# Kernel tuning notes

Hardware: AMD Instinct MI355X
Metric: run time of the kernel (lower is better)

Reference implementation:

```python
import jax, jax.numpy as jnp
import numpy as np

DIM = 256; DIM_HEAD = 32; HEADS = DIM // DIM_HEAD; WSZ = 8; D4 = DIM // 4
EPS = 1e-5
SCALE = DIM_HEAD ** -0.5


def _rel_pos_indices(wsz):
    pos = np.arange(wsz)
    grid = np.stack(np.meshgrid(pos, pos, indexing='ij')).reshape(2, -1).T  # (w*w, 2)
    rel = grid[:, None] - grid[None, :] + wsz - 1
    return jnp.asarray((rel * np.array([2 * wsz - 1, 1])).sum(-1))  # (w*w, w*w)


def _ln(x, g, b):
    m = x.mean(-1, keepdims=True)
    v = jnp.var(x, axis=-1, keepdims=True)
    return (x - m) / jnp.sqrt(v + EPS) * g + b


def setup_inputs() -> dict:
    key = jax.random.key(0)
    ks = jax.random.split(key, 8)
    inner = HEADS * DIM_HEAD
    def n(k, shape, s=0.02):
        return jax.random.normal(k, shape, dtype=jnp.float32) * s
    return {
        "x": jax.random.normal(ks[0], (2, DIM, 256, 256), dtype=jnp.float32),
        "norm_g": jnp.ones((1, DIM, 1, 1), jnp.float32),
        "norm_b": jnp.zeros((1, DIM, 1, 1), jnp.float32),
        "w_qkv": n(ks[1], (3 * inner, DIM)),
        "w_out": n(ks[2], (DIM, inner)),
        "b_out": jnp.zeros((DIM,), jnp.float32),
        "dpb_w1": n(ks[3], (D4, 2), 0.5), "dpb_b1": jnp.zeros((D4,), jnp.float32),
        "dpb_g1": jnp.ones((D4,), jnp.float32), "dpb_beta1": jnp.zeros((D4,), jnp.float32),
        "dpb_w2": n(ks[4], (D4, D4), 0.1), "dpb_b2": jnp.zeros((D4,), jnp.float32),
        "dpb_g2": jnp.ones((D4,), jnp.float32), "dpb_beta2": jnp.zeros((D4,), jnp.float32),
        "dpb_w3": n(ks[5], (D4, D4), 0.1), "dpb_b3": jnp.zeros((D4,), jnp.float32),
        "dpb_g3": jnp.ones((D4,), jnp.float32), "dpb_beta3": jnp.zeros((D4,), jnp.float32),
        "dpb_w4": n(ks[6], (1, D4), 0.1), "dpb_b4": jnp.zeros((1,), jnp.float32),
    }


def reference(x, norm_g, norm_b, w_qkv, w_out, b_out,
              dpb_w1, dpb_b1, dpb_g1, dpb_beta1,
              dpb_w2, dpb_b2, dpb_g2, dpb_beta2,
              dpb_w3, dpb_b3, dpb_g3, dpb_beta3,
              dpb_w4, dpb_b4):
    B, D, H, W = x.shape
    nh, nw = H // WSZ, W // WSZ
    # channel-first LayerNorm (stats over dim=1, biased variance)
    mean = x.mean(axis=1, keepdims=True)
    var = jnp.var(x, axis=1, keepdims=True)
    xn = (x - mean) / jnp.sqrt(var + EPS) * norm_g + norm_b
    # 'short' windowing: b d (h s1) (w s2) -> (b h w) d (s1 s2)
    xw = xn.reshape(B, D, nh, WSZ, nw, WSZ).transpose(0, 2, 4, 1, 3, 5)
    xw = xw.reshape(B * nh * nw, D, WSZ * WSZ)
    # 1x1 conv QKV == matmul over channel dim
    qkv = jnp.einsum('ed,bdn->ben', w_qkv, xw)
    q, k, v = jnp.split(qkv, 3, axis=1)
    to_heads = lambda t: t.reshape(-1, HEADS, DIM_HEAD, WSZ * WSZ).transpose(0, 1, 3, 2)
    q, k, v = to_heads(q) * SCALE, to_heads(k), to_heads(v)
    sim = jnp.einsum('bhid,bhjd->bhij', q, k)  # [Bw, H, 64, 64]
    # dynamic position bias MLP over relative coordinates in [-wsz, wsz]
    pos = jnp.arange(-WSZ, WSZ + 1, dtype=x.dtype)
    rel = jnp.stack(jnp.meshgrid(pos, pos, indexing='ij')).reshape(2, -1).T  # ((2w+1)^2, 2)
    h1 = jax.nn.relu(_ln(rel @ dpb_w1.T + dpb_b1, dpb_g1, dpb_beta1))
    h2 = jax.nn.relu(_ln(h1 @ dpb_w2.T + dpb_b2, dpb_g2, dpb_beta2))
    h3 = jax.nn.relu(_ln(h2 @ dpb_w3.T + dpb_b3, dpb_g3, dpb_beta3))
    biases = (h3 @ dpb_w4.T + dpb_b4)[:, 0]
    sim = sim + biases[_rel_pos_indices(WSZ)]
    attn = jax.nn.softmax(sim, axis=-1)
    out = jnp.einsum('bhij,bhjd->bhid', attn, v)
    # b h (x y) d -> b (h d) (x y)
    out = out.transpose(0, 1, 3, 2).reshape(-1, HEADS * DIM_HEAD, WSZ * WSZ)
    out = jnp.einsum('de,ben->bdn', w_out, out) + b_out[None, :, None]
    # (b h w) d s1 s2 -> b d (h s1) (w s2)
    out = out.reshape(B, nh, nw, D, WSZ, WSZ).transpose(0, 3, 1, 4, 2, 5).reshape(B, D, H, W)
    return out
```

## Files before the change

kernel.cpp:

```cpp
#include <hip/hip_runtime.h>


typedef __attribute__((ext_vector_type(8))) short bf16x8;
typedef __attribute__((ext_vector_type(4))) short bf16x4;
typedef __attribute__((ext_vector_type(4))) float f32x4;

#define LOG2E    1.44269504088896f
#define QK_SCALE 0.17677669529663687f

__device__ __forceinline__ short f2b(float f) {
  union { float f; unsigned u; } v; v.f = f;
  unsigned r = v.u + 0x7FFFu + ((v.u >> 16) & 1u);
  return (short)(r >> 16);
}

__device__ __forceinline__ unsigned pk2(float a, float b) {
  union { float f; unsigned u; } ua, ub; ua.f = a; ub.f = b;
#if __has_builtin(__builtin_amdgcn_perm)
  return __builtin_amdgcn_perm(ub.u + 0x8000u, ua.u + 0x8000u, 0x07060302u);
#else
  return ((ua.u + 0x8000u) >> 16) | ((ub.u + 0x8000u) & 0xFFFF0000u);
#endif
}

__device__ __forceinline__ bf16x8 mk8(unsigned a, unsigned b, unsigned c, unsigned d) {
  union { unsigned u[4]; bf16x8 v; } x; x.u[0] = a; x.u[1] = b; x.u[2] = c; x.u[3] = d;
  return x.v;
}
__device__ __forceinline__ bf16x4 mk4(unsigned a, unsigned b) {
  union { unsigned u[2]; bf16x4 v; } x; x.u[0] = a; x.u[1] = b; return x.v;
}

__device__ __forceinline__ f32x4 mfma16(bf16x4 a, bf16x4 b, f32x4 c) {
#if __has_builtin(__builtin_amdgcn_mfma_f32_16x16x16bf16_1k)
  return __builtin_amdgcn_mfma_f32_16x16x16bf16_1k(a, b, c, 0, 0, 0);
#else
  f32x4 d;
  asm volatile("v_mfma_f32_16x16x16_bf16 %0, %1, %2, %3"
               : "=&v"(d) : "v"(a), "v"(b), "v"(c));
  return d;
#endif
}

__global__ __launch_bounds__(256)
void wconv_kernel(const float* __restrict__ wqkv, const float* __restrict__ wout,
                  short* __restrict__ wq_t, short* __restrict__ wo_t) {
  int t = (blockIdx.x * 256 + threadIdx.x) * 8;
  if (t < 196608) {
    int blk = t >> 9, l = (t & 511) >> 3;
    int et = blk >> 3, kt = blk & 7;
    int e = et * 16 + (l & 15);
    int d = kt * 32 + (l >> 4) * 8;
    const float* src = wqkv + e * 256 + d;
    float sc = (e < 256) ? QK_SCALE * LOG2E : 1.0f;
    bf16x8 pk;
    #pragma unroll
    for (int el = 0; el < 8; ++el) pk[el] = f2b(src[el] * sc);
    *(bf16x8*)(wq_t + t) = pk;
  } else if (t < 262144) {
    int o = t - 196608;
    int blk = o >> 9, l = (o & 511) >> 3;
    int dt = blk >> 3, kt = blk & 7;
    int dout = dt * 16 + (l & 15);
    int e = kt * 32 + (l >> 4) * 8;
    const float* src = wout + dout * 256 + e;
    bf16x8 pk;
    #pragma unroll
    for (int el = 0; el < 8; ++el) pk[el] = f2b(src[el]);
    *(bf16x8*)(wo_t + o) = pk;
  }
}

__device__ __forceinline__ float wave_sum64(float v) {
  v += __shfl_xor(v, 1);  v += __shfl_xor(v, 2);  v += __shfl_xor(v, 4);
  v += __shfl_xor(v, 8);  v += __shfl_xor(v, 16); v += __shfl_xor(v, 32);
  return v;
}

__global__ __launch_bounds__(64)
void dpb_kernel(const float* __restrict__ w1, const float* __restrict__ b1,
                const float* __restrict__ g1, const float* __restrict__ be1,
                const float* __restrict__ w2, const float* __restrict__ b2,
                const float* __restrict__ g2, const float* __restrict__ be2,
                const float* __restrict__ w3, const float* __restrict__ b3,
                const float* __restrict__ g3, const float* __restrict__ be3,
                const float* __restrict__ w4, const float* __restrict__ b4,
                float* __restrict__ sb) {
  __shared__ float h[64];
  __shared__ float wbuf[4096];
  const int f = threadIdx.x;
  const int pos = blockIdx.x;
  const float py = (float)(pos / 17) - 8.0f;
  const float px = (float)(pos % 17) - 8.0f;

  float a = py * w1[2 * f] + px * w1[2 * f + 1] + b1[f];
  {
    float m = wave_sum64(a) * (1.f / 64.f);
    float d = a - m;
    float var = wave_sum64(d * d) * (1.f / 64.f);
    a = fmaxf(d * rsqrtf(var + 1e-5f) * g1[f] + be1[f], 0.f);
  }
  h[f] = a;
  __threadfence_block();

  #pragma unroll 8
  for (int k = 0; k < 64; ++k) wbuf[k * 64 + f] = w2[k * 64 + f];
  __threadfence_block();
  float acc = b2[f];
  #pragma unroll 8
  for (int k = 0; k < 64; ++k) {
    int g = (k + f) & 63;
    acc += wbuf[f * 64 + g] * h[g];
  }
  {
    float m = wave_sum64(acc) * (1.f / 64.f);
    float d = acc - m;
    float var = wave_sum64(d * d) * (1.f / 64.f);
    acc = fmaxf(d * rsqrtf(var + 1e-5f) * g2[f] + be2[f], 0.f);
  }
  __threadfence_block();
  h[f] = acc;
  __threadfence_block();

  #pragma unroll 8
  for (int k = 0; k < 64; ++k) wbuf[k * 64 + f] = w3[k * 64 + f];
  __threadfence_block();
  float acc3 = b3[f];
  #pragma unroll 8
  for (int k = 0; k < 64; ++k) {
    int g = (k + f) & 63;
    acc3 += wbuf[f * 64 + g] * h[g];
  }
  {
    float m = wave_sum64(acc3) * (1.f / 64.f);
    float d = acc3 - m;
    float var = wave_sum64(d * d) * (1.f / 64.f);
    acc3 = fmaxf(d * rsqrtf(var + 1e-5f) * g3[f] + be3[f], 0.f);
  }
  float o = wave_sum64(w4[f] * acc3);
  if (f == 0) sb[pos] = o + b4[0];
}

__global__ __launch_bounds__(512)
void expand_kernel(const float* __restrict__ sb, float* __restrict__ tblf) {
  int idx = blockIdx.x * 512 + threadIdx.x;
  int it = idx >> 10, jt = (idx >> 8) & 3, ln = (idx >> 2) & 63, jj = idx & 3;
  int rr = ln & 15, gg = ln >> 4;
  int i = it * 16 + rr;
  int j = jt * 16 + gg * 4 + jj;
  int dy = (i >> 3) - (j >> 3) + 7;
  int dx = (i & 7) - (j & 7) + 7;
  tblf[idx] = sb[dy * 15 + dx] * LOG2E;
}

#define SM_XA   0
#define SM_PS   65536
#define SM_SIZE 73728
#define XASWZ(p) ((((p) & 7) << 4) ^ ((((p) >> 3) & 3) << 7))

__global__ __launch_bounds__(512)
void attn_kernel(const float* __restrict__ x, const float* __restrict__ gnorm,
                 const float* __restrict__ bnorm, const short* __restrict__ wq_t,
                 const short* __restrict__ wo_t, const float* __restrict__ bout,
                 const float* __restrict__ tblf, float* __restrict__ out) {
  __shared__ __align__(16) char smem[SM_SIZE];
  const int t = threadIdx.x;
  const int lane = t & 63;
  const int w = t >> 6;
  const int r = lane & 15;
  const int gq = lane >> 4;

  const int bid = blockIdx.x;
  const int b   = bid >> 9;
  const int wh  = (bid >> 4) & 31;
  const int ww2 = bid & 15;
  const int R = wh * 8, C = ww2 * 16;

  const int n = lane;
  const int d0 = w * 32;
  float* PS = (float*)(smem + SM_PS);
  float xv[2][32];
  #pragma unroll
  for (int h = 0; h < 2; ++h) {
    const float* xb = x + (((size_t)(b * 256 + d0)) << 16) +
                      (R + 4 * h + (n >> 4)) * 256 + C + (n & 15);
    float s1 = 0.f, s2v = 0.f;
    #pragma unroll
    for (int i = 0; i < 32; ++i) {
      float v = xb[(size_t)i << 16];
      xv[h][i] = v; s1 += v; s2v += v * v;
    }
    PS[h * 1024 + w * 64 + n] = s1;
    PS[h * 1024 + 512 + w * 64 + n] = s2v;
  }
  __syncthreads();
  #pragma unroll
  for (int h = 0; h < 2; ++h) {
    float a = 0.f, q2 = 0.f;
    #pragma unroll
    for (int dg = 0; dg < 8; ++dg) {
      a  += PS[h * 1024 + dg * 64 + n];
      q2 += PS[h * 1024 + 512 + dg * 64 + n];
    }
    float mean = a * (1.f / 256.f);
    float var = q2 * (1.f / 256.f) - mean * mean;
    float rstd = rsqrtf(var + 1e-5f);
    int p2 = (4 * h + (n >> 4)) * 16 + (n & 15);
    #pragma unroll
    for (int c = 0; c < 4; ++c) {
      float xn[8];
      #pragma unroll
      for (int e = 0; e < 8; ++e) {
        int d = d0 + c * 8 + e;
        xn[e] = (xv[h][c * 8 + e] - mean) * rstd * gnorm[d] + bnorm[d];
      }
      *(bf16x8*)(smem + SM_XA + (p2 << 9) + ((((d0 + c * 8) << 1)) ^ XASWZ(p2))) =
          mk8(pk2(xn[0], xn[1]), pk2(xn[2], xn[3]), pk2(xn[4], xn[5]), pk2(xn[6], xn[7]));
    }
  }
  __syncthreads();

  const f32x4 vzero = {0.f, 0.f, 0.f, 0.f};

  #define QKV_SWAP(PP, ACC)                                                     \
    {                                                                           \
      _Pragma("unroll")                                                         \
      for (int nt = 0; nt < 2; ++nt)                                            \
        _Pragma("unroll")                                                       \
        for (int t4 = 0; t4 < 4; ++t4) ACC[nt][t4] = vzero;                     \
      _Pragma("unroll")                                                         \
      for (int kt = 0; kt < 8; ++kt) {                                          \
        bf16x8 bfr0 = *(const bf16x8*)(wq_t + (((((PP) * 16 + w * 2 + 0) * 8 + kt) << 9) + lane * 8)); \
        bf16x8 bfr1 = *(const bf16x8*)(wq_t + (((((PP) * 16 + w * 2 + 1) * 8 + kt) << 9) + lane * 8)); \
        bf16x8 afr[4];                                                          \
        _Pragma("unroll")                                                       \
        for (int t4 = 0; t4 < 4; ++t4) {                                        \
          int p2 = (t4 * 2 + (r >> 3)) * 16 + wl * 8 + (r & 7);                 \
          afr[t4] = *(const bf16x8*)(smem + SM_XA + (p2 << 9) + ((((kt * 32 + gq * 8) << 1)) ^ XASWZ(p2))); \
        }                                                                       \
        _Pragma("unroll")                                                       \
        for (int t4 = 0; t4 < 4; ++t4) {                                        \
          ACC[0][t4] = __builtin_amdgcn_mfma_f32_16x16x32_bf16(bfr0, afr[t4], ACC[0][t4], 0, 0, 0); \
          ACC[1][t4] = __builtin_amdgcn_mfma_f32_16x16x32_bf16(bfr1, afr[t4], ACC[1][t4], 0, 0, 0); \
        }                                                                       \
      }                                                                         \
    }

  f32x4 o2[2][2][4];
  #pragma unroll
  for (int wl = 0; wl < 2; ++wl) {
    bf16x4 kpk[2][4], qpk[2][4];
    {
      f32x4 acc[2][4];
      QKV_SWAP(1, acc);
      #pragma unroll
      for (int kb = 0; kb < 2; ++kb)
        #pragma unroll
        for (int jt = 0; jt < 4; ++jt)
          kpk[kb][jt] = mk4(pk2(acc[kb][jt][0], acc[kb][jt][1]),
                            pk2(acc[kb][jt][2], acc[kb][jt][3]));
    }
    {
      f32x4 acc[2][4];
      QKV_SWAP(0, acc);
      #pragma unroll
      for (int kb = 0; kb < 2; ++kb)
        #pragma unroll
        for (int it = 0; it < 4; ++it)
          qpk[kb][it] = mk4(pk2(acc[kb][it][0], acc[kb][it][1]),
                            pk2(acc[kb][it][2], acc[kb][it][3]));
    }
    bf16x4 va8[4][2];
    {
      f32x4 vacc[4][2];
      #pragma unroll
      for (int mt = 0; mt < 4; ++mt)
        #pragma unroll
        for (int nt = 0; nt < 2; ++nt) vacc[mt][nt] = vzero;
      #pragma unroll
      for (int kt = 0; kt < 8; ++kt) {
        bf16x8 bfr0 = *(const bf16x8*)(wq_t + ((((2 * 16 + w * 2 + 0) * 8 + kt) << 9) + lane * 8));
        bf16x8 bfr1 = *(const bf16x8*)(wq_t + ((((2 * 16 + w * 2 + 1) * 8 + kt) << 9) + lane * 8));
        bf16x8 afr[4];
        #pragma unroll
        for (int mt = 0; mt < 4; ++mt) {
          int p2 = (mt * 2 + (r >> 3)) * 16 + wl * 8 + (r & 7);
          afr[mt] = *(const bf16x8*)(smem + SM_XA + (p2 << 9) + ((((kt * 32 + gq * 8) << 1)) ^ XASWZ(p2)));
        }
        #pragma unroll
        for (int mt = 0; mt < 4; ++mt) {
          vacc[mt][0] = __builtin_amdgcn_mfma_f32_16x16x32_bf16(afr[mt], bfr0, vacc[mt][0], 0, 0, 0);
          vacc[mt][1] = __builtin_amdgcn_mfma_f32_16x16x32_bf16(afr[mt], bfr1, vacc[mt][1], 0, 0, 0);
        }
      }
      #pragma unroll
      for (int mt = 0; mt < 4; ++mt)
        #pragma unroll
        for (int nt = 0; nt < 2; ++nt)
          va8[mt][nt] = mk4(pk2(vacc[mt][nt][0], vacc[mt][nt][1]),
                            pk2(vacc[mt][nt][2], vacc[mt][nt][3]));
    }

    #pragma unroll
    for (int nt = 0; nt < 2; ++nt)
      #pragma unroll
      for (int it = 0; it < 4; ++it) o2[wl][nt][it] = vzero;
    __builtin_amdgcn_s_setprio(1);
    #pragma unroll
    for (int it = 0; it < 4; ++it) {
      f32x4 sc[4];
      #pragma unroll
      for (int jt = 0; jt < 4; ++jt) {
        sc[jt] = mfma16(kpk[0][jt], qpk[0][it], vzero);
        sc[jt] = mfma16(kpk[1][jt], qpk[1][it], sc[jt]);
      }
      float m0 = -1e30f;
      #pragma unroll
      for (int jt = 0; jt < 4; ++jt) {
        f32x4 bj = *(const f32x4*)(tblf + (((it * 4 + jt) * 64 + lane) << 2));
        #pragma unroll
        for (int jj = 0; jj < 4; ++jj) {
          sc[jt][jj] += bj[jj];
          m0 = fmaxf(m0, sc[jt][jj]);
        }
      }
      m0 = fmaxf(m0, __shfl_xor(m0, 16));
      m0 = fmaxf(m0, __shfl_xor(m0, 32));
      float sum = 0.f;
      #pragma unroll
      for (int jt = 0; jt < 4; ++jt)
        #pragma unroll
        for (int jj = 0; jj < 4; ++jj) {
          float e = exp2f(sc[jt][jj] - m0);
          sc[jt][jj] = e; sum += e;
        }
      sum += __shfl_xor(sum, 16);
      sum += __shfl_xor(sum, 32);
      float pinv = 1.0f / sum;
      bf16x4 ppk[4];
      #pragma unroll
      for (int jt = 0; jt < 4; ++jt)
        ppk[jt] = mk4(pk2(sc[jt][0] * pinv, sc[jt][1] * pinv),
                      pk2(sc[jt][2] * pinv, sc[jt][3] * pinv));
      #pragma unroll
      for (int mt = 0; mt < 4; ++mt)
        #pragma unroll
        for (int nt = 0; nt < 2; ++nt)
          o2[wl][nt][it] = mfma16(va8[mt][nt], ppk[mt], o2[wl][nt][it]);
    }
    __builtin_amdgcn_s_setprio(0);
  }
  __syncthreads();

  #pragma unroll
  for (int wl = 0; wl < 2; ++wl)
    #pragma unroll
    for (int nt = 0; nt < 2; ++nt)
      #pragma unroll
      for (int it = 0; it < 4; ++it) {
        int pw = it * 16 + r;
        int p2 = ((pw >> 3) << 4) + (wl << 3) + (pw & 7);
        int e = (w << 5) + (nt << 4) + (gq << 2);
        *(bf16x4*)(smem + SM_XA + (p2 << 9) + (((e << 1)) ^ XASWZ(p2))) =
            mk4(pk2(o2[wl][nt][it][0], o2[wl][nt][it][1]),
                pk2(o2[wl][nt][it][2], o2[wl][nt][it][3]));
      }
  __syncthreads();

  float bov[2];
  bov[0] = bout[w * 32 + r];
  bov[1] = bout[w * 32 + 16 + r];

  #pragma unroll
  for (int ck = 0; ck < 2; ++ck) {
    f32x4 c3[4][2];
    #pragma unroll
    for (int mt = 0; mt < 4; ++mt)
      #pragma unroll
      for (int nt = 0; nt < 2; ++nt) c3[mt][nt] = vzero;
    __builtin_amdgcn_s_setprio(1);
    #pragma unroll
    for (int kt = 0; kt < 8; ++kt) {
      bf16x8 woB[2];
      #pragma unroll
      for (int nt = 0; nt < 2; ++nt)
        woB[nt] = *(const bf16x8*)(wo_t + ((((w * 2 + nt) * 8 + kt) << 9) + lane * 8));
      bf16x8 af[4];
      #pragma unroll
      for (int mt = 0; mt < 4; ++mt) {
        int p2 = ck * 64 + mt * 16 + r;
        af[mt] = *(const bf16x8*)(smem + SM_XA + (p2 << 9) + ((((kt * 32 + gq * 8) << 1)) ^ XASWZ(p2)));
      }
      #pragma unroll
      for (int mt = 0; mt < 4; ++mt)
        #pragma unroll
        for (int nt = 0; nt < 2; ++nt)
          c3[mt][nt] = __builtin_amdgcn_mfma_f32_16x16x32_bf16(af[mt], woB[nt], c3[mt][nt], 0, 0, 0);
    }
    __builtin_amdgcn_s_setprio(0);
    #pragma unroll
    for (int mt = 0; mt < 4; ++mt)
      #pragma unroll
      for (int nt = 0; nt < 2; ++nt) {
        int dout = w * 32 + nt * 16 + r;
        int row = ck * 4 + mt;
        f32x4 v = c3[mt][nt];
        v[0] += bov[nt]; v[1] += bov[nt]; v[2] += bov[nt]; v[3] += bov[nt];
        *(f32x4*)(out + (((size_t)(b * 256 + dout)) << 16) + (R + row) * 256 + C + gq * 4) = v;
      }
  }
  #undef QKV_SWAP
}

extern "C" void kernel_launch(void* const* d_in, const int* in_sizes, int n_in,
                              void* d_out, int out_size, void* d_ws, size_t ws_size,
                              hipStream_t stream) {
  const float* x     = (const float*)d_in[0];
  const float* gnorm = (const float*)d_in[1];
  const float* bnorm = (const float*)d_in[2];
  const float* wqkv  = (const float*)d_in[3];
  const float* wout  = (const float*)d_in[4];
  const float* bout  = (const float*)d_in[5];
  const float* w1  = (const float*)d_in[6];
  const float* b1  = (const float*)d_in[7];
  const float* g1  = (const float*)d_in[8];
  const float* be1 = (const float*)d_in[9];
  const float* w2  = (const float*)d_in[10];
  const float* b2  = (const float*)d_in[11];
  const float* g2  = (const float*)d_in[12];
  const float* be2 = (const float*)d_in[13];
  const float* w3  = (const float*)d_in[14];
  const float* b3  = (const float*)d_in[15];
  const float* g3  = (const float*)d_in[16];
  const float* be3 = (const float*)d_in[17];
  const float* w4  = (const float*)d_in[18];
  const float* b4  = (const float*)d_in[19];

  short* wq_t = (short*)d_ws;
  short* wo_t = wq_t + 196608;
  float* sb   = (float*)((char*)d_ws + 524288);
  float* tblf = (float*)((char*)d_ws + 528384);

  wconv_kernel<<<dim3(128), dim3(256), 0, stream>>>(wqkv, wout, wq_t, wo_t);
  dpb_kernel<<<dim3(289), dim3(64), 0, stream>>>(
      w1, b1, g1, be1, w2, b2, g2, be2, w3, b3, g3, be3, w4, b4, sb);
  expand_kernel<<<dim3(8), dim3(512), 0, stream>>>(sb, tblf);

  attn_kernel<<<dim3(1024), dim3(512), 0, stream>>>(
      x, gnorm, bnorm, wq_t, wo_t, bout, tblf, (float*)d_out);
}
```

Before: 193.5 us.

## Split LayerNorm into separate kernel staging swizzled bf16 tiles in workspace

Moves the channel LayerNorm and bf16 packing out of the attention kernel into a dedicated ln_kernel that writes each block's swizzled 64KB tile to workspace. The attention kernel then just copies that tile into shared memory with vector loads. This is meant to cut register pressure and the long latency of the strided fp32 loads inside the attention kernel. In exchange it adds a round trip of an extra 64MB intermediate through memory and a second launch. It falls back to the fused path when the workspace is too small.

```diff
diff --git a/kernel.cpp b/kernel.cpp
--- a/kernel.cpp
+++ b/kernel.cpp
@@ -159,10 +159,67 @@
 #define XASWZ(p) ((((p) & 7) << 4) ^ ((((p) >> 3) & 3) << 7))
 
 __global__ __launch_bounds__(512)
+void ln_kernel(const float* __restrict__ x, const float* __restrict__ gnorm,
+               const float* __restrict__ bnorm, char* __restrict__ xng) {
+  __shared__ __align__(16) float PS[2048];
+  const int t = threadIdx.x;
+  const int lane = t & 63;
+  const int w = t >> 6;
+  const int n = lane;
+  const int d0 = w * 32;
+
+  const int bid = blockIdx.x;
+  const int b   = bid >> 9;
+  const int wh  = (bid >> 4) & 31;
+  const int ww2 = bid & 15;
+  const int R = wh * 8, C = ww2 * 16;
+  char* dst = xng + (size_t)bid * 65536;
+
+  #pragma unroll 1
+  for (int h = 0; h < 2; ++h) {
+    const float* xb = x + (((size_t)(b * 256 + d0)) << 16) +
+                      (R + 4 * h + (n >> 4)) * 256 + C + (n & 15);
+    float xv[32];
+    float s1 = 0.f, s2v = 0.f;
+    #pragma unroll
+    for (int i = 0; i < 32; ++i) {
+      float v = xb[(size_t)i << 16];
+      xv[i] = v; s1 += v; s2v += v * v;
+    }
+    PS[(h & 1) * 1024 + w * 64 + n] = s1;
+    PS[(h & 1) * 1024 + 512 + w * 64 + n] = s2v;
+    __syncthreads();
+    float a = 0.f, q2 = 0.f;
+    #pragma unroll
+    for (int dg = 0; dg < 8; ++dg) {
+      a  += PS[(h & 1) * 1024 + dg * 64 + n];
+      q2 += PS[(h & 1) * 1024 + 512 + dg * 64 + n];
+    }
+    float mean = a * (1.f / 256.f);
+    float var = q2 * (1.f / 256.f) - mean * mean;
+    float rstd = rsqrtf(var + 1e-5f);
+    int p2 = (4 * h + (n >> 4)) * 16 + (n & 15);
+    #pragma unroll
+    for (int c = 0; c < 4; ++c) {
+      float xn[8];
+      #pragma unroll
+      for (int e = 0; e < 8; ++e) {
+        int d = d0 + c * 8 + e;
+        xn[e] = (xv[c * 8 + e] - mean) * rstd * gnorm[d] + bnorm[d];
+      }
+      *(bf16x8*)(dst + (p2 << 9) + ((((d0 + c * 8) << 1)) ^ XASWZ(p2))) =
+          mk8(pk2(xn[0], xn[1]), pk2(xn[2], xn[3]), pk2(xn[4], xn[5]), pk2(xn[6], xn[7]));
+    }
+  }
+}
+
+template <int STAGED>
+__global__ __launch_bounds__(512)
 void attn_kernel(const float* __restrict__ x, const float* __restrict__ gnorm,
                  const float* __restrict__ bnorm, const short* __restrict__ wq_t,
                  const short* __restrict__ wo_t, const float* __restrict__ bout,
-                 const float* __restrict__ tblf, float* __restrict__ out) {
+                 const float* __restrict__ tblf, const char* __restrict__ xng,
+                 float* __restrict__ out) {
   __shared__ __align__(16) char smem[SM_SIZE];
   const int t = threadIdx.x;
   const int lane = t & 63;
@@ -176,49 +233,59 @@
   const int ww2 = bid & 15;
   const int R = wh * 8, C = ww2 * 16;
 
-  const int n = lane;
-  const int d0 = w * 32;
-  float* PS = (float*)(smem + SM_PS);
-  float xv[2][32];
-  #pragma unroll
-  for (int h = 0; h < 2; ++h) {
-    const float* xb = x + (((size_t)(b * 256 + d0)) << 16) +
-                      (R + 4 * h + (n >> 4)) * 256 + C + (n & 15);
-    float s1 = 0.f, s2v = 0.f;
-    #pragma unroll
-    for (int i = 0; i < 32; ++i) {
-      float v = xb[(size_t)i << 16];
-      xv[h][i] = v; s1 += v; s2v += v * v;
-    }
-    PS[h * 1024 + w * 64 + n] = s1;
-    PS[h * 1024 + 512 + w * 64 + n] = s2v;
-  }
-  __syncthreads();
-  #pragma unroll
-  for (int h = 0; h < 2; ++h) {
-    float a = 0.f, q2 = 0.f;
-    #pragma unroll
-    for (int dg = 0; dg < 8; ++dg) {
-      a  += PS[h * 1024 + dg * 64 + n];
-      q2 += PS[h * 1024 + 512 + dg * 64 + n];
-    }
-    float mean = a * (1.f / 256.f);
-    float var = q2 * (1.f / 256.f) - mean * mean;
-    float rstd = rsqrtf(var + 1e-5f);
-    int p2 = (4 * h + (n >> 4)) * 16 + (n & 15);
-    #pragma unroll
-    for (int c = 0; c < 4; ++c) {
-      float xn[8];
-      #pragma unroll
-      for (int e = 0; e < 8; ++e) {
-        int d = d0 + c * 8 + e;
-        xn[e] = (xv[h][c * 8 + e] - mean) * rstd * gnorm[d] + bnorm[d];
-      }
-      *(bf16x8*)(smem + SM_XA + (p2 << 9) + ((((d0 + c * 8) << 1)) ^ XASWZ(p2))) =
-          mk8(pk2(xn[0], xn[1]), pk2(xn[2], xn[3]), pk2(xn[4], xn[5]), pk2(xn[6], xn[7]));
-    }
-  }
-  __syncthreads();
+  if constexpr (STAGED) {
+    const char* src = xng + (size_t)bid * 65536;
+    #pragma unroll
+    for (int i = 0; i < 8; ++i) {
+      int off = i * 8192 + t * 16;
+      *(f32x4*)(smem + SM_XA + off) = *(const f32x4*)(src + off);
+    }
+    __syncthreads();
+  } else {
+    const int n = lane;
+    const int d0 = w * 32;
+    float* PS = (float*)(smem + SM_PS);
+    float xv[2][32];
+    #pragma unroll
+    for (int h = 0; h < 2; ++h) {
+      const float* xb = x + (((size_t)(b * 256 + d0)) << 16) +
+                        (R + 4 * h + (n >> 4)) * 256 + C + (n & 15);
+      float s1 = 0.f, s2v = 0.f;
+      #pragma unroll
+      for (int i = 0; i < 32; ++i) {
+        float v = xb[(size_t)i << 16];
+        xv[h][i] = v; s1 += v; s2v += v * v;
+      }
+      PS[h * 1024 + w * 64 + n] = s1;
+      PS[h * 1024 + 512 + w * 64 + n] = s2v;
+    }
+    __syncthreads();
+    #pragma unroll
+    for (int h = 0; h < 2; ++h) {
+      float a = 0.f, q2 = 0.f;
+      #pragma unroll
+      for (int dg = 0; dg < 8; ++dg) {
+        a  += PS[h * 1024 + dg * 64 + n];
+        q2 += PS[h * 1024 + 512 + dg * 64 + n];
+      }
+      float mean = a * (1.f / 256.f);
+      float var = q2 * (1.f / 256.f) - mean * mean;
+      float rstd = rsqrtf(var + 1e-5f);
+      int p2 = (4 * h + (n >> 4)) * 16 + (n & 15);
+      #pragma unroll
+      for (int c = 0; c < 4; ++c) {
+        float xn[8];
+        #pragma unroll
+        for (int e = 0; e < 8; ++e) {
+          int d = d0 + c * 8 + e;
+          xn[e] = (xv[h][c * 8 + e] - mean) * rstd * gnorm[d] + bnorm[d];
+        }
+        *(bf16x8*)(smem + SM_XA + (p2 << 9) + ((((d0 + c * 8) << 1)) ^ XASWZ(p2))) =
+            mk8(pk2(xn[0], xn[1]), pk2(xn[2], xn[3]), pk2(xn[4], xn[5]), pk2(xn[6], xn[7]));
+      }
+    }
+    __syncthreads();
+  }
 
   const f32x4 vzero = {0.f, 0.f, 0.f, 0.f};
 
@@ -440,12 +507,20 @@
   short* wo_t = wq_t + 196608;
   float* sb   = (float*)((char*)d_ws + 524288);
   float* tblf = (float*)((char*)d_ws + 528384);
+  char*  xng  = (char*)d_ws + (1 << 20);
 
   wconv_kernel<<<dim3(128), dim3(256), 0, stream>>>(wqkv, wout, wq_t, wo_t);
   dpb_kernel<<<dim3(289), dim3(64), 0, stream>>>(
       w1, b1, g1, be1, w2, b2, g2, be2, w3, b3, g3, be3, w4, b4, sb);
   expand_kernel<<<dim3(8), dim3(512), 0, stream>>>(sb, tblf);
 
-  attn_kernel<<<dim3(1024), dim3(512), 0, stream>>>(
-      x, gnorm, bnorm, wq_t, wo_t, bout, tblf, (float*)d_out);
-}
+  const size_t need = (size_t)(1 << 20) + (size_t)1024 * 65536;
+  if (ws_size >= need) {
+    ln_kernel<<<dim3(1024), dim3(512), 0, stream>>>(x, gnorm, bnorm, xng);
+    attn_kernel<1><<<dim3(1024), dim3(512), 0, stream>>>(
+        x, gnorm, bnorm, wq_t, wo_t, bout, tblf, xng, (float*)d_out);
+  } else {
+    attn_kernel<0><<<dim3(1024), dim3(512), 0, stream>>>(
+        x, gnorm, bnorm, wq_t, wo_t, bout, tblf, xng, (float*)d_out);
+  }
+}
```

After: 223.6 us. +15.6%, slower.
